# Performance work log

Hardware: AMD Instinct MI355X
Metric: run time of the kernel (lower is better)

Reference implementation:

```python
import jax, jax.numpy as jnp
import numpy as np

B, S, D, H = 4, 2048, 1024, 16
HD = D // H  # head_dim = 64

def setup_inputs() -> dict:
    key = jax.random.key(0)
    ks = jax.random.split(key, 11)
    s = 1.0 / np.sqrt(D)
    return {
        "query": jax.random.normal(ks[0], (B, S, D), jnp.float32),
        "key": jax.random.normal(ks[1], (B, S, D), jnp.float32),
        "value": jax.random.normal(ks[2], (B, S, D), jnp.float32),
        "Wq": jax.random.normal(ks[3], (D, D), jnp.float32) * s,
        "bq": jnp.zeros((D,), jnp.float32),
        "Wk": jax.random.normal(ks[4], (D, D), jnp.float32) * s,
        "bk": jnp.zeros((D,), jnp.float32),
        "Wv": jax.random.normal(ks[5], (D, D), jnp.float32) * s,
        "bv": jnp.zeros((D,), jnp.float32),
        "Wo": jax.random.normal(ks[6], (D, D), jnp.float32) * s,
        "bo": jnp.zeros((D,), jnp.float32),
    }

def reference(query, key, value, Wq, bq, Wk, bk, Wv, bv, Wo, bo):
    b = query.shape[0]
    # linear projections, then split heads -> [b, H, S, HD]
    Q = (query @ Wq + bq).reshape(b, -1, H, HD).transpose(0, 2, 1, 3)
    K = (key @ Wk + bk).reshape(b, -1, H, HD).transpose(0, 2, 1, 3)
    V = (value @ Wv + bv).reshape(b, -1, H, HD).transpose(0, 2, 1, 3)
    energy = jnp.einsum('bhqd,bhkd->bhqk', Q, K) / np.sqrt(HD)  # [b,H,S,S]
    attn = jax.nn.softmax(energy, axis=-1)
    x = jnp.einsum('bhqk,bhkd->bhqd', attn, V)
    x = x.transpose(0, 2, 1, 3).reshape(b, -1, H * HD)
    return x @ Wo + bo
```

## Files before the change

### kernel.cpp

```cpp
#include <hip/hip_runtime.h>
#include <math.h>

constexpr int Bb = 4, Ss = 2048, Dd = 1024, Hh = 16, HDd = 64;

typedef __attribute__((ext_vector_type(8))) short short8;
typedef __attribute__((ext_vector_type(4))) float floatx4;
typedef __attribute__((ext_vector_type(16))) float floatx16;
typedef __attribute__((ext_vector_type(4))) unsigned int uint4v;

__device__ inline unsigned short bf16r(float f) {
    unsigned int u = __builtin_bit_cast(unsigned int, f);
    u += 0x7fffu + ((u >> 16) & 1u);
    return (unsigned short)(u >> 16);
}
__device__ inline unsigned int cvtpk(float lo, float hi) {
    unsigned int r;
    asm("v_cvt_pk_bf16_f32 %0, %1, %2" : "=v"(r) : "v"(lo), "v"(hi));
    return r;
}
__device__ inline uint4v pk8(float4 x, float4 y) {
    uint4v r = {cvtpk(x.x, x.y), cvtpk(x.z, x.w), cvtpk(y.x, y.y), cvtpk(y.z, y.w)};
    return r;
}

__device__ inline void gld16(const void* g, void* l) {
    __builtin_amdgcn_global_load_lds((const __attribute__((address_space(1))) void*)g,
                                     (__attribute__((address_space(3))) void*)l, 16, 0, 0);
}

__device__ inline floatx4 mfma16(short8 a, short8 b, floatx4 c) {
    return __builtin_amdgcn_mfma_f32_16x16x32_bf16(a, b, c, 0, 0, 0);
}
__device__ inline floatx16 mfma32(short8 a, short8 b, floatx16 c) {
    return __builtin_amdgcn_mfma_f32_32x32x16_bf16(a, b, c, 0, 0, 0);
}

#define LOG2E 1.4426950408889634f
#define EXP2_SHIFT 17.312340490667562f

__global__ __launch_bounds__(256)
void conv_w_kernel(const float* __restrict__ Wq, const float* __restrict__ Wk,
                   const float* __restrict__ Wv, const float* __restrict__ Wo,
                   unsigned short* __restrict__ Wt)
{
    int z = blockIdx.z;
    const float* W = z == 0 ? Wq : z == 1 ? Wk : z == 2 ? Wv : Wo;
    float scale = z == 0 ? 0.125f * LOG2E : 1.0f;
    unsigned short* out = Wt + (size_t)z * 1024 * 1024;

    int r0 = blockIdx.x * 64;
    int c0 = blockIdx.y * 64;
    int t = threadIdx.x;
    int oc = (t & 3) * 16;
    int orow = c0 + (t >> 2);

    float v[16];
    #pragma unroll
    for (int j = 0; j < 16; ++j)
        v[j] = W[(size_t)(r0 + oc + j) * 1024 + orow] * scale;

    unsigned int pk[8];
    #pragma unroll
    for (int j = 0; j < 8; ++j) pk[j] = cvtpk(v[2 * j], v[2 * j + 1]);

    uint4v w0 = {pk[0], pk[1], pk[2], pk[3]};
    uint4v w1 = {pk[4], pk[5], pk[6], pk[7]};
    *(uint4v*)(out + (size_t)orow * 1024 + r0 + oc) = w0;
    *(uint4v*)(out + (size_t)orow * 1024 + r0 + oc + 8) = w1;
}

__global__ __launch_bounds__(256)
void conv_bias_kernel(const float* __restrict__ bq, float* __restrict__ bqs)
{
    int idx = blockIdx.x * 256 + threadIdx.x;
    if (idx < 1024) bqs[idx] = bq[idx] * 0.125f * LOG2E;
}

__global__ __launch_bounds__(256)
void qkv_gemm_kernel(const float* __restrict__ qin, const float* __restrict__ kin,
                     const float* __restrict__ vin,
                     const unsigned short* __restrict__ Wt,
                     const float* __restrict__ bqs, const float* __restrict__ bk,
                     const float* __restrict__ bv,
                     unsigned short* __restrict__ Qb, unsigned short* __restrict__ Kb,
                     unsigned short* __restrict__ Vb)
{
    int z = blockIdx.z;
    const float* A = z == 0 ? qin : z == 1 ? kin : vin;
    const unsigned short* W = Wt + (size_t)z * 1024 * 1024;
    const float* bias = z == 0 ? bqs : z == 1 ? bk : bv;
    unsigned short* O = z == 0 ? Qb : z == 1 ? Kb : Vb;

    __shared__ __align__(16) char qsm[40960];
    char* Ab0 = qsm;
    char* Ab1 = qsm + 8192;
    char* pB0 = qsm + 16384;
    char* pB1 = qsm + 24576;
    char* pB2 = qsm + 32768;

    int tid = threadIdx.x, lane = tid & 63, w = tid >> 6;
    int wr = w >> 1, wc = w & 1;
    int fr = lane & 15, fg = lane >> 4;
    int m0 = blockIdx.x * 128, n0 = blockIdx.y * 128;

    const float* Arow = A + (size_t)(m0 + (tid >> 1)) * 1024 + (tid & 1) * 16;
    const int aWX = (tid & 4) << 2;
    const int aRdoB = (((wr * 64 + fr) * 32 + fg * 8) * 2) ^ ((fr & 2) << 3);
    const int bRdoB = ((wc * 64 + fr) * 32 + fg * 8) * 2;

    floatx4 acc[4][4] = {};
    float4 arE0, arE1, arE2, arE3, arO0, arO1, arO2, arO3;

#define LOADA(s, kt) { const float* Ar_ = Arow + (kt) * 32;                     \
        s##0 = *(const float4*)(Ar_);      s##1 = *(const float4*)(Ar_ + 4);    \
        s##2 = *(const float4*)(Ar_ + 8);  s##3 = *(const float4*)(Ar_ + 12); }
#define GLB(kt, dst) {                                                          \
        const unsigned short* g0_ = W + (size_t)(n0 + (tid >> 2)) * 1024 + (kt) * 32 + (tid & 3) * 8;          \
        gld16(g0_, (dst) + (size_t)(w * 64) * 16);                              \
        const unsigned short* g1_ = W + (size_t)(n0 + ((tid + 256) >> 2)) * 1024 + (kt) * 32 + (tid & 3) * 8;  \
        gld16(g1_, (dst) + (size_t)(256 + w * 64) * 16); }
#define WRITEA(s, dst) { char* pb_ = (dst) + tid * 32;                          \
        *(uint4v*)(pb_ + aWX) = pk8(s##0, s##1);                                \
        *(uint4v*)(pb_ + (aWX ^ 16)) = pk8(s##2, s##3); }
#define COMP(Acur, Bcur) { short8 af_[4], bf_[4];                               \
        _Pragma("unroll")                                                       \
        for (int mi = 0; mi < 4; ++mi) af_[mi] = *(const short8*)((Acur) + aRdoB + mi * 1024); \
        _Pragma("unroll")                                                       \
        for (int ni = 0; ni < 4; ++ni) bf_[ni] = *(const short8*)((Bcur) + bRdoB + ni * 1024); \
        _Pragma("unroll")                                                       \
        for (int mi = 0; mi < 4; ++mi)                                          \
            _Pragma("unroll")                                                   \
            for (int ni = 0; ni < 4; ++ni)                                      \
                acc[mi][ni] = mfma16(af_[mi], bf_[ni], acc[mi][ni]); }
#define FENCE6 { asm volatile("s_waitcnt vmcnt(6) lgkmcnt(0)" ::: "memory");    \
        __builtin_amdgcn_s_barrier(); __builtin_amdgcn_sched_barrier(0); }
#define FENCE0 { asm volatile("s_waitcnt vmcnt(0) lgkmcnt(0)" ::: "memory");    \
        __builtin_amdgcn_s_barrier(); __builtin_amdgcn_sched_barrier(0); }

    LOADA(arE, 0); GLB(0, pB0);
    LOADA(arO, 1); GLB(1, pB1);
    WRITEA(arE, Ab0);
    FENCE6;

    for (int p = 0; p < 15; ++p) {
        int kt = 2 * p;
        LOADA(arE, kt + 2); GLB(kt + 2, pB2);
        COMP(Ab0, pB0);
        WRITEA(arO, Ab1);
        FENCE6;
        LOADA(arO, kt + 3); GLB(kt + 3, pB0);
        COMP(Ab1, pB1);
        WRITEA(arE, Ab0);
        FENCE6;
        char* t_ = pB0; pB0 = pB2; pB2 = pB1; pB1 = t_;
    }

    COMP(Ab0, pB0);
    WRITEA(arO, Ab1);
    FENCE0;
    COMP(Ab1, pB1);
    __syncthreads();

#undef LOADA
#undef GLB
#undef WRITEA
#undef COMP
#undef FENCE6
#undef FENCE0

    float bvv[4];
    #pragma unroll
    for (int ni = 0; ni < 4; ++ni) bvv[ni] = bias[n0 + wc * 64 + ni * 16 + fr];

    if (z == 2) {
        unsigned short* T = (unsigned short*)(qsm) + (size_t)w * 4608;
        #pragma unroll
        for (int mi = 0; mi < 4; ++mi)
            #pragma unroll
            for (int ni = 0; ni < 4; ++ni) {
                int hdl = ni * 16 + fr;
                int sl  = mi * 16 + fg * 4;
                uint2 u2;
                u2.x = cvtpk(acc[mi][ni][0] + bvv[ni], acc[mi][ni][1] + bvv[ni]);
                u2.y = cvtpk(acc[mi][ni][2] + bvv[ni], acc[mi][ni][3] + bvv[ni]);
                *(uint2*)(T + hdl * 72 + sl) = u2;
            }
        int h  = (n0 + wc * 64) >> 6;
        int Ms = m0 + wr * 64;
        int b_ = Ms >> 11, sbase = Ms & 2047;
        unsigned short* Od = O + (((size_t)(b_ * 16 + h) * 64) << 11) + sbase;
        int rg = lane >> 3, sc = lane & 7;
        #pragma unroll
        for (int j = 0; j < 8; ++j) {
            int row = j * 8 + rg;
            uint4v t = *(const uint4v*)(T + row * 72 + sc * 8);
            *(uint4v*)(Od + ((size_t)row << 11) + sc * 8) = t;
        }
    } else {
        #pragma unroll
        for (int mi = 0; mi < 4; ++mi)
            #pragma unroll
            for (int ni = 0; ni < 4; ++ni) {
                int n = n0 + wc * 64 + ni * 16 + fr;
                int h = n >> 6, hd = n & 63;
                #pragma unroll
                for (int i = 0; i < 4; ++i) {
                    int m = m0 + wr * 64 + mi * 16 + fg * 4 + i;
                    int b_ = m >> 11, s = m & 2047;
                    float val = acc[mi][ni][i] + bvv[ni];
                    O[(((size_t)(b_ * 16 + h) * 2048 + s) << 6) + hd] = bf16r(val);
                }
            }
    }
}

__global__ __launch_bounds__(256)
void attn_kernel(const unsigned short* __restrict__ Qb, const unsigned short* __restrict__ Kb,
                 const unsigned short* __restrict__ Vtb, unsigned short* __restrict__ Xb)
{
    __shared__ __align__(16) char smem[32768];

    int pphys = blockIdx.x + (blockIdx.y << 4) + (blockIdx.z << 8);
    int L = (pphys & 7) * 128 + (pphys >> 3);
    int qt = L & 15;
    int h  = (L >> 4) & 15;
    int b  = L >> 8;

    int tid = threadIdx.x, lane = tid & 63, w = tid >> 6;
    int c = lane & 31, hi = lane >> 5;
    int q0 = qt * 128;
    size_t base = ((size_t)(b * 16 + h)) * 2048 * 64;
    const unsigned short* Qp = Qb + base + (size_t)(q0 + w * 32) * 64;
    const unsigned short* Kp = Kb + base;
    const unsigned short* Vp = Vtb + base;

    short8 qfr[4];
    #pragma unroll
    for (int ks = 0; ks < 4; ++ks)
        qfr[ks] = *(const short8*)(Qp + (size_t)c * 64 + ks * 16 + hi * 8);

    floatx16 acc_o[2] = {};
    floatx16 acc_l = {};
    uint4v onesu = {0x3F803F80u, 0x3F803F80u, 0x3F803F80u, 0x3F803F80u};
    short8 onesb = __builtin_bit_cast(short8, onesu);

    int p0 = tid & 7;
    int r0 = tid >> 3;
    int r1 = r0 + 32;
    int g0 = p0 ^ (r0 & 7);

    auto STAGE = [&](int kt, char* Kd, char* Vd) {
        gld16(Kp + ((size_t)(kt * 64 + r0) << 6) + g0 * 8, Kd + (size_t)tid * 16);
        gld16(Kp + ((size_t)(kt * 64 + r1) << 6) + g0 * 8, Kd + (size_t)(tid + 256) * 16);
        gld16(Vp + ((size_t)r0 << 11) + kt * 64 + g0 * 8, Vd + (size_t)tid * 16);
        gld16(Vp + ((size_t)r1 << 11) + kt * 64 + g0 * 8, Vd + (size_t)(tid + 256) * 16);
    };

    STAGE(0, smem, smem + 8192);
    __syncthreads();

    for (int kt = 0; kt < 32; ++kt) {
        char* Kl = smem + (kt & 1) * 16384;
        char* Vl = Kl + 8192;
        if (kt + 1 < 32) {
            char* Kn = smem + ((kt + 1) & 1) * 16384;
            STAGE(kt + 1, Kn, Kn + 8192);
        }

        #pragma unroll
        for (int kvt = 0; kvt < 2; ++kvt) {
            floatx16 st;
            #pragma unroll
            for (int r = 0; r < 16; ++r) st[r] = -EXP2_SHIFT;

            __builtin_amdgcn_s_setprio(1);
            #pragma unroll
            for (int ks = 0; ks < 4; ++ks) {
                int row = kvt * 32 + c;
                short8 kf = *(const short8*)(Kl + row * 128 +
                                             ((ks * 32 + hi * 16) ^ ((row & 7) << 4)));
                st = mfma32(kf, qfr[ks], st);
            }
            __builtin_amdgcn_s_setprio(0);

            float p[16];
            #pragma unroll
            for (int r = 0; r < 16; ++r)
                p[r] = __builtin_amdgcn_exp2f(st[r]);
            unsigned int j[8];
            #pragma unroll
            for (int t2 = 0; t2 < 8; ++t2)
                j[t2] = cvtpk(p[2 * t2], p[2 * t2 + 1]);
            asm volatile("v_permlane32_swap_b32 %0, %1" : "+v"(j[0]), "+v"(j[2]));
            asm volatile("v_permlane32_swap_b32 %0, %1" : "+v"(j[1]), "+v"(j[3]));
            asm volatile("v_permlane32_swap_b32 %0, %1" : "+v"(j[4]), "+v"(j[6]));
            asm volatile("v_permlane32_swap_b32 %0, %1" : "+v"(j[5]), "+v"(j[7]));
            uint4v pa0 = {j[0], j[1], j[2], j[3]};
            uint4v pa1 = {j[4], j[5], j[6], j[7]};
            short8 paA = __builtin_bit_cast(short8, pa0);
            short8 paB = __builtin_bit_cast(short8, pa1);

            __builtin_amdgcn_s_setprio(1);
            #pragma unroll
            for (int kvs2 = 0; kvs2 < 2; ++kvs2) {
                int kstep = kvt * 2 + kvs2;
                short8 pa = kvs2 ? paB : paA;
                #pragma unroll
                for (int dvt = 0; dvt < 2; ++dvt) {
                    int dv = dvt * 32 + c;
                    short8 vf = *(const short8*)(Vl + dv * 128 +
                                                 ((kstep * 32 + hi * 16) ^ ((dv & 7) << 4)));
                    acc_o[dvt] = mfma32(pa, vf, acc_o[dvt]);
                }
            }
            acc_l = mfma32(paA, onesb, acc_l);
            acc_l = mfma32(paB, onesb, acc_l);
            __builtin_amdgcn_s_setprio(0);
        }
        __syncthreads();
    }

    unsigned short* Ot = (unsigned short*)smem;

    #pragma unroll
    for (int r = 0; r < 16; ++r) {
        int rowq = (r & 3) + 8 * (r >> 2) + 4 * hi;
        float inv = 1.0f / acc_l[r];
        int ql = w * 32 + rowq;
        Ot[ql * 64 + c]      = bf16r(acc_o[0][r] * inv);
        Ot[ql * 64 + 32 + c] = bf16r(acc_o[1][r] * inv);
    }
    __syncthreads();

    {
        int row = tid >> 1, half = tid & 1;
        const unsigned short* src = Ot + row * 64 + half * 32;
        unsigned short* dst = Xb + ((size_t)b * 2048 + q0 + row) * 1024
                                 + h * 64 + half * 32;
        uint4v v0 = *(const uint4v*)(src);
        uint4v v1 = *(const uint4v*)(src + 8);
        uint4v v2 = *(const uint4v*)(src + 16);
        uint4v v3 = *(const uint4v*)(src + 24);
        *(uint4v*)(dst) = v0;
        *(uint4v*)(dst + 8) = v1;
        *(uint4v*)(dst + 16) = v2;
        *(uint4v*)(dst + 24) = v3;
    }
}

__global__ __launch_bounds__(256)
void out_gemm_kernel(const unsigned short* __restrict__ Xb,
                     const unsigned short* __restrict__ Wto,
                     const float* __restrict__ bo, float* __restrict__ out)
{
    __shared__ __align__(16) char osm[32768];
    unsigned short* Asm0 = (unsigned short*)(osm);
    unsigned short* Bsm0 = (unsigned short*)(osm + 8192);
    unsigned short* Asm1 = (unsigned short*)(osm + 16384);
    unsigned short* Bsm1 = (unsigned short*)(osm + 24576);

    int tid = threadIdx.x, lane = tid & 63, w = tid >> 6;
    int wr = w >> 1, wc = w & 1;
    int fr = lane & 15, fg = lane >> 4;
    int m0 = blockIdx.x * 128, n0 = blockIdx.y * 128;

    const int aRdo = (wr * 64 + fr) * 32 + fg * 8;
    const int bRdo = (wc * 64 + fr) * 32 + fg * 8;

    floatx4 acc[4][4] = {};

    auto STAGE = [&](int k0, unsigned short* Ad, unsigned short* Bd) {
        #pragma unroll
        for (int it = 0; it < 2; ++it) {
            int cA = tid + it * 256;
            const unsigned short* ga = Xb + (size_t)(m0 + (cA >> 2)) * 1024 + k0 + (cA & 3) * 8;
            gld16(ga, (char*)Ad + (size_t)(it * 256 + w * 64) * 16);
            const unsigned short* gb = Wto + (size_t)(n0 + (cA >> 2)) * 1024 + k0 + (cA & 3) * 8;
            gld16(gb, (char*)Bd + (size_t)(it * 256 + w * 64) * 16);
        }
    };

    STAGE(0, Asm0, Bsm0);
    __syncthreads();

    for (int kt = 0; kt < 32; ++kt) {
        unsigned short* Acur = (kt & 1) ? Asm1 : Asm0;
        unsigned short* Bcur = (kt & 1) ? Bsm1 : Bsm0;
        if (kt < 31)
            STAGE((kt + 1) * 32, (kt & 1) ? Asm0 : Asm1, (kt & 1) ? Bsm0 : Bsm1);

        short8 af[4], bf[4];
        #pragma unroll
        for (int mi = 0; mi < 4; ++mi) af[mi] = *(const short8*)(Acur + aRdo + mi * 16 * 32);
        #pragma unroll
        for (int ni = 0; ni < 4; ++ni) bf[ni] = *(const short8*)(Bcur + bRdo + ni * 16 * 32);
        #pragma unroll
        for (int mi = 0; mi < 4; ++mi)
            #pragma unroll
            for (int ni = 0; ni < 4; ++ni)
                acc[mi][ni] = mfma16(af[mi], bf[ni], acc[mi][ni]);
        __syncthreads();
    }

    float bvv[4];
    #pragma unroll
    for (int ni = 0; ni < 4; ++ni) bvv[ni] = bo[n0 + wc * 64 + ni * 16 + fr];

    #pragma unroll
    for (int mi = 0; mi < 4; ++mi)
        #pragma unroll
        for (int ni = 0; ni < 4; ++ni) {
            int n = n0 + wc * 64 + ni * 16 + fr;
            #pragma unroll
            for (int i = 0; i < 4; ++i) {
                int m = m0 + wr * 64 + mi * 16 + fg * 4 + i;
                out[(size_t)m * 1024 + n] = acc[mi][ni][i] + bvv[ni];
            }
        }
}

extern "C" void kernel_launch(void* const* d_in, const int* in_sizes, int n_in,
                              void* d_out, int out_size, void* d_ws, size_t ws_size,
                              hipStream_t stream)
{
    const float* qin = (const float*)d_in[0];
    const float* kin = (const float*)d_in[1];
    const float* vin = (const float*)d_in[2];
    const float* Wq  = (const float*)d_in[3];
    const float* bq  = (const float*)d_in[4];
    const float* Wk  = (const float*)d_in[5];
    const float* bk  = (const float*)d_in[6];
    const float* Wv  = (const float*)d_in[7];
    const float* bv  = (const float*)d_in[8];
    const float* Wo  = (const float*)d_in[9];
    const float* bo  = (const float*)d_in[10];
    float* out = (float*)d_out;

    char* ws = (char*)d_ws;
    unsigned short* Wt  = (unsigned short*)(ws);
    float*          bqs = (float*)(ws + 8388608);
    unsigned short* Qb  = (unsigned short*)(ws + 8392704);
    unsigned short* Kb  = (unsigned short*)(ws + 8392704 + 16777216);
    unsigned short* Vb  = (unsigned short*)(ws + 8392704 + 2 * 16777216);
    unsigned short* Xb  = (unsigned short*)(ws + 8392704 + 3 * 16777216);

    conv_w_kernel<<<dim3(16, 16, 4), 256, 0, stream>>>(Wq, Wk, Wv, Wo, Wt);
    conv_bias_kernel<<<dim3(4), 256, 0, stream>>>(bq, bqs);
    qkv_gemm_kernel<<<dim3(64, 8, 3), 256, 0, stream>>>(qin, kin, vin, Wt, bqs, bk, bv,
                                                        Qb, Kb, Vb);
    attn_kernel<<<dim3(16, 16, 4), 256, 0, stream>>>(Qb, Kb, Vb, Xb);
    out_gemm_kernel<<<dim3(64, 8), 256, 0, stream>>>(Xb, Wt + 3145728, bo, out);
}
```

Before: 217.7 us.

## Stream fp32 A tiles directly to LDS and convert to bf16 at fragment load

The QKV projection GEMM now loads the fp32 activation tile straight into LDS with global_load_lds and an XOR swizzle. The bf16 conversion moves from the register staging and write step to the point where MFMA fragments are read from LDS. A triple-buffered A and double-buffered B pipeline with split vmcnt/lgkmcnt fences replaces the old register-prefetch scheme, aiming to remove VGPR staging and LDS write instructions from the main loop. In exchange LDS use grows to 64 KB, which may limit occupancy, and each A fragment is converted again on every read. A barrier was also added before the V transpose store.

```diff
diff --git a/kernel.cpp b/kernel.cpp
--- a/kernel.cpp
+++ b/kernel.cpp
@@ -16,10 +16,6 @@
 __device__ inline unsigned int cvtpk(float lo, float hi) {
     unsigned int r;
     asm("v_cvt_pk_bf16_f32 %0, %1, %2" : "=v"(r) : "v"(lo), "v"(hi));
-    return r;
-}
-__device__ inline uint4v pk8(float4 x, float4 y) {
-    uint4v r = {cvtpk(x.x, x.y), cvtpk(x.z, x.w), cvtpk(y.x, y.y), cvtpk(y.z, y.w)};
     return r;
 }
 
@@ -87,86 +83,91 @@
 {
     int z = blockIdx.z;
     const float* A = z == 0 ? qin : z == 1 ? kin : vin;
-    const unsigned short* W = Wt + (size_t)z * 1024 * 1024;
+    const unsigned short* W = Wt + (size_t)z * 1048576;
     const float* bias = z == 0 ? bqs : z == 1 ? bk : bv;
     unsigned short* O = z == 0 ? Qb : z == 1 ? Kb : Vb;
 
-    __shared__ __align__(16) char qsm[40960];
-    char* Ab0 = qsm;
-    char* Ab1 = qsm + 8192;
-    char* pB0 = qsm + 16384;
-    char* pB1 = qsm + 24576;
-    char* pB2 = qsm + 32768;
+    __shared__ __align__(16) char qsm[65536];
+    char* Aa0 = qsm;
+    char* Aa1 = qsm + 16384;
+    char* Aa2 = qsm + 32768;
+    char* Bb0 = qsm + 49152;
+    char* Bb1 = qsm + 57344;
 
     int tid = threadIdx.x, lane = tid & 63, w = tid >> 6;
     int wr = w >> 1, wc = w & 1;
     int fr = lane & 15, fg = lane >> 4;
     int m0 = blockIdx.x * 128, n0 = blockIdx.y * 128;
 
-    const float* Arow = A + (size_t)(m0 + (tid >> 1)) * 1024 + (tid & 1) * 16;
-    const int aWX = (tid & 4) << 2;
-    const int aRdoB = (((wr * 64 + fr) * 32 + fg * 8) * 2) ^ ((fr & 2) << 3);
+    int arow_base = w * 32 + (lane >> 3);
+    int asrc_col = (((lane & 7) ^ ((lane >> 3) & 7)) << 4) >> 2;
     const int bRdoB = ((wc * 64 + fr) * 32 + fg * 8) * 2;
 
     floatx4 acc[4][4] = {};
-    float4 arE0, arE1, arE2, arE3, arO0, arO1, arO2, arO3;
-
-#define LOADA(s, kt) { const float* Ar_ = Arow + (kt) * 32;                     \
-        s##0 = *(const float4*)(Ar_);      s##1 = *(const float4*)(Ar_ + 4);    \
-        s##2 = *(const float4*)(Ar_ + 8);  s##3 = *(const float4*)(Ar_ + 12); }
+
+#define ISSUEA(kt, dst) {                                                       \
+    _Pragma("unroll")                                                           \
+    for (int j_ = 0; j_ < 4; ++j_) {                                            \
+        const float* g_ = A + (size_t)(m0 + arow_base + j_ * 8) * 1024          \
+                            + (kt) * 32 + asrc_col;                             \
+        gld16(g_, (dst) + (size_t)((w << 8) + (j_ << 6) + lane) * 16);          \
+    }}
 #define GLB(kt, dst) {                                                          \
-        const unsigned short* g0_ = W + (size_t)(n0 + (tid >> 2)) * 1024 + (kt) * 32 + (tid & 3) * 8;          \
-        gld16(g0_, (dst) + (size_t)(w * 64) * 16);                              \
-        const unsigned short* g1_ = W + (size_t)(n0 + ((tid + 256) >> 2)) * 1024 + (kt) * 32 + (tid & 3) * 8;  \
-        gld16(g1_, (dst) + (size_t)(256 + w * 64) * 16); }
-#define WRITEA(s, dst) { char* pb_ = (dst) + tid * 32;                          \
-        *(uint4v*)(pb_ + aWX) = pk8(s##0, s##1);                                \
-        *(uint4v*)(pb_ + (aWX ^ 16)) = pk8(s##2, s##3); }
-#define COMP(Acur, Bcur) { short8 af_[4], bf_[4];                               \
+    const unsigned short* g0_ = W + (size_t)(n0 + (tid >> 2)) * 1024 + (kt) * 32 + (tid & 3) * 8;          \
+    gld16(g0_, (dst) + (size_t)(w * 64) * 16);                                  \
+    const unsigned short* g1_ = W + (size_t)(n0 + ((tid + 256) >> 2)) * 1024 + (kt) * 32 + (tid & 3) * 8;  \
+    gld16(g1_, (dst) + (size_t)(256 + w * 64) * 16); }
+#define COMP(Ac, Bc) { short8 af_[4], bf_[4];                                   \
+    _Pragma("unroll")                                                           \
+    for (int mi = 0; mi < 4; ++mi) {                                            \
+        int row_ = wr * 64 + mi * 16 + fr;                                      \
+        int xb_ = (row_ & 7) << 4;                                              \
+        floatx4 al_ = *(const floatx4*)((Ac) + row_ * 128 + ((fg * 32) ^ xb_)); \
+        floatx4 ah_ = *(const floatx4*)((Ac) + row_ * 128 + ((fg * 32 + 16) ^ xb_)); \
+        uint4v u_ = {cvtpk(al_[0], al_[1]), cvtpk(al_[2], al_[3]),              \
+                     cvtpk(ah_[0], ah_[1]), cvtpk(ah_[2], ah_[3])};             \
+        af_[mi] = __builtin_bit_cast(short8, u_);                               \
+    }                                                                           \
+    _Pragma("unroll")                                                           \
+    for (int ni = 0; ni < 4; ++ni) bf_[ni] = *(const short8*)((Bc) + bRdoB + ni * 1024); \
+    _Pragma("unroll")                                                           \
+    for (int mi = 0; mi < 4; ++mi)                                              \
         _Pragma("unroll")                                                       \
-        for (int mi = 0; mi < 4; ++mi) af_[mi] = *(const short8*)((Acur) + aRdoB + mi * 1024); \
-        _Pragma("unroll")                                                       \
-        for (int ni = 0; ni < 4; ++ni) bf_[ni] = *(const short8*)((Bcur) + bRdoB + ni * 1024); \
-        _Pragma("unroll")                                                       \
-        for (int mi = 0; mi < 4; ++mi)                                          \
-            _Pragma("unroll")                                                   \
-            for (int ni = 0; ni < 4; ++ni)                                      \
-                acc[mi][ni] = mfma16(af_[mi], bf_[ni], acc[mi][ni]); }
-#define FENCE6 { asm volatile("s_waitcnt vmcnt(6) lgkmcnt(0)" ::: "memory");    \
-        __builtin_amdgcn_s_barrier(); __builtin_amdgcn_sched_barrier(0); }
-#define FENCE0 { asm volatile("s_waitcnt vmcnt(0) lgkmcnt(0)" ::: "memory");    \
-        __builtin_amdgcn_s_barrier(); __builtin_amdgcn_sched_barrier(0); }
-
-    LOADA(arE, 0); GLB(0, pB0);
-    LOADA(arO, 1); GLB(1, pB1);
-    WRITEA(arE, Ab0);
-    FENCE6;
-
-    for (int p = 0; p < 15; ++p) {
-        int kt = 2 * p;
-        LOADA(arE, kt + 2); GLB(kt + 2, pB2);
-        COMP(Ab0, pB0);
-        WRITEA(arO, Ab1);
-        FENCE6;
-        LOADA(arO, kt + 3); GLB(kt + 3, pB0);
-        COMP(Ab1, pB1);
-        WRITEA(arE, Ab0);
-        FENCE6;
-        char* t_ = pB0; pB0 = pB2; pB2 = pB1; pB1 = t_;
-    }
-
-    COMP(Ab0, pB0);
-    WRITEA(arO, Ab1);
-    FENCE0;
-    COMP(Ab1, pB1);
+        for (int ni = 0; ni < 4; ++ni)                                          \
+            acc[mi][ni] = mfma16(af_[mi], bf_[ni], acc[mi][ni]); }
+#define FV10 { asm volatile("s_waitcnt vmcnt(10)" ::: "memory");                \
+    __builtin_amdgcn_s_barrier(); __builtin_amdgcn_sched_barrier(0); }
+#define FV6  { asm volatile("s_waitcnt vmcnt(6)" ::: "memory");                 \
+    __builtin_amdgcn_s_barrier(); __builtin_amdgcn_sched_barrier(0); }
+#define FV0  { asm volatile("s_waitcnt vmcnt(0)" ::: "memory");                 \
+    __builtin_amdgcn_s_barrier(); __builtin_amdgcn_sched_barrier(0); }
+#define FL   { asm volatile("s_waitcnt lgkmcnt(0)" ::: "memory");               \
+    __builtin_amdgcn_s_barrier(); __builtin_amdgcn_sched_barrier(0); }
+
+    ISSUEA(0, Aa0); GLB(0, Bb0); ISSUEA(1, Aa1);
+
+    for (int p = 0; p < 5; ++p) {
+        int kt = 6 * p;
+        GLB(kt + 1, Bb1); ISSUEA(kt + 2, Aa2); FV10; COMP(Aa0, Bb0); FL;
+        GLB(kt + 2, Bb0); ISSUEA(kt + 3, Aa0); FV10; COMP(Aa1, Bb1); FL;
+        GLB(kt + 3, Bb1); ISSUEA(kt + 4, Aa1); FV10; COMP(Aa2, Bb0); FL;
+        GLB(kt + 4, Bb0); ISSUEA(kt + 5, Aa2); FV10; COMP(Aa0, Bb1); FL;
+        GLB(kt + 5, Bb1); ISSUEA(kt + 6, Aa0); FV10; COMP(Aa1, Bb0); FL;
+        GLB(kt + 6, Bb0); ISSUEA(kt + 7, Aa1); FV10; COMP(Aa2, Bb1); FL;
+    }
+
+    GLB(31, Bb1);
+    FV6; COMP(Aa0, Bb0); FL;
+    FV0; COMP(Aa1, Bb1);
     __syncthreads();
 
-#undef LOADA
+#undef ISSUEA
 #undef GLB
-#undef WRITEA
 #undef COMP
-#undef FENCE6
-#undef FENCE0
+#undef FV10
+#undef FV6
+#undef FV0
+#undef FL
 
     float bvv[4];
     #pragma unroll
@@ -185,6 +186,7 @@
                 u2.y = cvtpk(acc[mi][ni][2] + bvv[ni], acc[mi][ni][3] + bvv[ni]);
                 *(uint2*)(T + hdl * 72 + sl) = u2;
             }
+        __syncthreads();
         int h  = (n0 + wc * 64) >> 6;
         int Ms = m0 + wr * 64;
         int b_ = Ms >> 11, sbase = Ms & 2047;
```

New measurement: 205.2 us, median of 2. 5.7% less time.
